# Optimization experiments

Hardware: AMD Instinct MI355X
Metric: run time of the kernel (lower is better)

Reference implementation:

```python
import jax, jax.numpy as jnp
import numpy as np

B, S = 1, 4096
H, KV, D, HID = 8, 4, 256, 2304   # heads, kv heads, head_dim, hidden_size
G = H // KV                        # GQA group size
WINDOW = 1024                      # sliding window
THETA = 10000.0                    # rope_local_base_freq (sliding attention)
EPS = 1e-6
SCALE = 256.0 ** -0.5              # query_pre_attn_scalar ** -0.5


def rms_norm(x, w, eps=EPS):
    # Gemma3RMSNorm: fp32 rms over last dim, scale by (1 + weight)
    v = jnp.mean(jnp.square(x), axis=-1, keepdims=True)
    return x * jax.lax.rsqrt(v + eps) * (1.0 + w)


def rope(x, position_ids):
    # x: [B, S, N, D]; split-half rotation as in Gemma3RotaryEmbedding
    d = x.shape[-1]
    inv_freq = 1.0 / (THETA ** (jnp.arange(0, d, 2, dtype=jnp.float32) / d))  # [D/2]
    freqs = position_ids.astype(jnp.float32)[:, :, None] * inv_freq  # [B, S, D/2]
    cos = jnp.cos(freqs)[:, :, None, :]  # [B, S, 1, D/2]
    sin = jnp.sin(freqs)[:, :, None, :]
    x1, x2 = jnp.split(x, 2, axis=-1)
    return jnp.concatenate([x1 * cos - x2 * sin, x1 * sin + x2 * cos], axis=-1)


def setup_inputs() -> dict:
    key = jax.random.key(0)
    ks = jax.random.split(key, 6)
    n = lambda k, shp, sc: jax.random.normal(k, shp, dtype=jnp.float32) * sc
    return {
        "x": n(ks[0], (B, S, HID), 1.0),
        "position_ids": jnp.broadcast_to(jnp.arange(S, dtype=jnp.int32)[None, :], (B, S)),
        "wq": n(ks[1], (HID, H * D), 0.02),
        "wk": n(ks[2], (HID, KV * D), 0.02),
        "wv": n(ks[3], (HID, KV * D), 0.02),
        "wo": n(ks[4], (H * D, HID), 0.02),
        "q_norm_w": jnp.zeros((D,), dtype=jnp.float32),
        "k_norm_w": jnp.zeros((D,), dtype=jnp.float32),
    }


def reference(x, position_ids, wq, wk, wv, wo, q_norm_w, k_norm_w):
    b, s, _ = x.shape
    q = (x @ wq).reshape(b, s, H, D)
    k = (x @ wk).reshape(b, s, KV, D)
    v = (x @ wv).reshape(b, s, KV, D)

    # QK-RMSNorm over head_dim, then RoPE, then query scaling
    q = rms_norm(q, q_norm_w)
    k = rms_norm(k, k_norm_w)
    q = rope(q, position_ids)
    k = rope(k, position_ids)
    q = q * SCALE

    # GQA: group queries over shared KV heads. qg: [B, S, KV, G, D]
    qg = q.reshape(b, s, KV, G, D)
    scores = jnp.einsum('bqcgd,btcd->bcgqt', qg, k)  # [B, KV, G, S, S]

    # causal + sliding-window mask: t <= q and q - t < WINDOW
    pi = position_ids[:, :, None]  # query positions [B, S, 1]
    pj = position_ids[:, None, :]  # key positions   [B, 1, S]
    mask = (pj <= pi) & (pi - pj < WINDOW)  # [B, S, S]
    neg = jnp.finfo(scores.dtype).min
    scores = jnp.where(mask[:, None, None, :, :], scores, neg)

    probs = jax.nn.softmax(scores, axis=-1)
    out = jnp.einsum('bcgqt,btcd->bqcgd', probs, v).reshape(b, s, H * D)
    return out @ wo
```

## Files before the change

### kernel.cpp

```cpp
#include <hip/hip_runtime.h>
#include <stdint.h>

typedef unsigned short u16;
typedef __attribute__((ext_vector_type(8))) short bf16x8;
typedef __attribute__((ext_vector_type(4))) float f32x4;

#define S_LEN 4096
#define HID_DIM 2304
#define QKV_N 4096
#define AO_N 2048
#define HD 256
#define WIN 1024
#define QSCALE 0.0625f

static __device__ __forceinline__ u16 f2bf(float f) {
  union { float f; uint32_t u; } v; v.f = f;
  return (u16)((v.u + 0x7FFFu + ((v.u >> 16) & 1u)) >> 16);
}
static __device__ __forceinline__ float bf2f(u16 h) {
  union { uint32_t u; float f; } v; v.u = ((uint32_t)h) << 16;
  return v.f;
}

static __device__ __forceinline__ void gld16(const void* src, void* dst) {
  __builtin_amdgcn_global_load_lds((const __attribute__((address_space(1))) void*)src,
                                   (__attribute__((address_space(3))) void*)dst, 16, 0, 0);
}

#define BAR() __builtin_amdgcn_s_barrier()
#define LG0() asm volatile("s_waitcnt lgkmcnt(0)" ::: "memory")
#define VM6() asm volatile("s_waitcnt vmcnt(6)" ::: "memory")
#define VM5() asm volatile("s_waitcnt vmcnt(5)" ::: "memory")
#define VM4() asm volatile("s_waitcnt vmcnt(4)" ::: "memory")
#define VM3() asm volatile("s_waitcnt vmcnt(3)" ::: "memory")
#define VM2() asm volatile("s_waitcnt vmcnt(2)" ::: "memory")
#define VM0() asm volatile("s_waitcnt vmcnt(0)" ::: "memory")
#define PRIO1() __builtin_amdgcn_s_setprio(1)
#define PRIO0() __builtin_amdgcn_s_setprio(0)

__global__ __launch_bounds__(256) void k_cvt_bf16(const float* __restrict__ in,
                                                  u16* __restrict__ out, int n) {
  int i = (blockIdx.x * 256 + threadIdx.x) * 4;
  if (i >= n) return;
  float4 v = *(const float4*)(in + i);
  uint64_t p = (uint64_t)f2bf(v.x) | ((uint64_t)f2bf(v.y) << 16)
             | ((uint64_t)f2bf(v.z) << 32) | ((uint64_t)f2bf(v.w) << 48);
  *(uint64_t*)(out + i) = p;
}

__global__ __launch_bounds__(256) void k_sincos(const int* __restrict__ pos_ids,
                                                float* __restrict__ ctab,
                                                float* __restrict__ stab) {
  int idx = blockIdx.x * 256 + threadIdx.x;
  int s = idx >> 7, j = idx & 127;
  float ang = (float)pos_ids[s] * exp2f((float)j * (-13.287712379549449f / 128.0f));
  float sn, c;
  sincosf(ang, &sn, &c);
  ctab[idx] = c;
  stab[idx] = sn;
}

__global__ __launch_bounds__(256) void k_transpose_cvt(const float* __restrict__ in, int C,
                                                       u16* __restrict__ out, int out_stride,
                                                       int row_off) {
  __shared__ float tile[32][33];
  int c0 = blockIdx.x * 32, r0 = blockIdx.y * 32;
  int tx = threadIdx.x & 31, ty = threadIdx.x >> 5;
#pragma unroll
  for (int i = 0; i < 4; i++)
    tile[ty + i * 8][tx] = in[(size_t)(r0 + ty + i * 8) * C + c0 + tx];
  __syncthreads();
#pragma unroll
  for (int i = 0; i < 4; i++)
    out[(size_t)(row_off + c0 + ty + i * 8) * out_stride + r0 + tx] = f2bf(tile[tx][ty + i * 8]);
}

__global__ __launch_bounds__(256) void k_transpose_w(const float* __restrict__ wq,
                                                     const float* __restrict__ wk,
                                                     const float* __restrict__ wv,
                                                     u16* __restrict__ out) {
  int ct = blockIdx.x;
  int r0 = blockIdx.y * 32;
  const float* src;
  int C, c0;
  if (ct < 64) {
    src = wq; C = 2048; c0 = ct * 32;
  } else if (ct < 96) {
    src = wk; C = 1024; c0 = (ct - 64) * 32;
  } else {
    src = wv; C = 1024; c0 = (ct - 96) * 32;
  }
  __shared__ float tile[32][33];
  int tx = threadIdx.x & 31, ty = threadIdx.x >> 5;
#pragma unroll
  for (int i = 0; i < 4; i++)
    tile[ty + i * 8][tx] = src[(size_t)(r0 + ty + i * 8) * C + c0 + tx];
  __syncthreads();
#pragma unroll
  for (int i = 0; i < 4; i++)
    out[(size_t)(ct * 32 + ty + i * 8) * HID_DIM + r0 + tx] = f2bf(tile[tx][ty + i * 8]);
}

template <int MODE>
__global__ __launch_bounds__(512, 2) void k_gemm8p(const u16* __restrict__ A,
                                                   const u16* __restrict__ Bt,
                                                   void* __restrict__ Cout,
                                                   int M, int N, int K,
                                                   const float* __restrict__ ctab,
                                                   const float* __restrict__ stab,
                                                   const float* __restrict__ qnw,
                                                   const float* __restrict__ knw,
                                                   u16* __restrict__ vtb) {
  __shared__ u16 sA[2][256 * 64];
  __shared__ u16 sB[2][256 * 64];
  const int t = threadIdx.x, lane = t & 63, wave = t >> 6;
  const int wr = wave >> 2, wc = wave & 3;
  const int l15 = lane & 15, l4 = lane >> 4;
  const int nbn = N >> 8;
  const int cpx = gridDim.x >> 3;
  const int wg = ((int)blockIdx.x & 7) * cpx + ((int)blockIdx.x >> 3);
  const int bm = wg / nbn, bn = wg % nbn;
  const int NT = K >> 6;
  const int srow = lane >> 3;
  const int sslot = ((lane & 7) ^ srow) * 8;
  const u16* Abase = A + (size_t)(bm * 256) * K;
  const u16* Bbase = Bt + (size_t)(bn * 256) * K;
  f32x4 acc[8][4] = {};
  bf16x8 aF[4][2], b01[2][2], b23[2][2];

#define STG_A(BUF, HALF, KT) do {                                                 \
    _Pragma("unroll")                                                             \
    for (int c_ = 0; c_ < 2; c_++) {                                              \
      int rb_ = (HALF) * 128 + (wave * 2 + c_) * 8;                               \
      gld16(Abase + (size_t)(rb_ + srow) * K + ((KT) << 6) + sslot,               \
            &sA[BUF][rb_ * 64]);                                                  \
    }                                                                             \
  } while (0)
#define STG_B(BUF, HALF, KT) do {                                                 \
    _Pragma("unroll")                                                             \
    for (int c_ = 0; c_ < 2; c_++) {                                              \
      int rb_ = (HALF) * 128 + (wave * 2 + c_) * 8;                               \
      gld16(Bbase + (size_t)(rb_ + srow) * K + ((KT) << 6) + sslot,               \
            &sB[BUF][rb_ * 64]);                                                  \
    }                                                                             \
  } while (0)
#define LDA(BUF, M_, KK)                                                          \
  (*(const bf16x8*)&sA[BUF][((M_) * 32 + wr * 16 + l15) * 64 +                    \
                            ((((KK) << 2) + l4) ^ (l15 & 7)) * 8])
#define LDB(BUF, N_, KK)                                                          \
  (*(const bf16x8*)&sB[BUF][((N_) * 64 + wc * 16 + l15) * 64 +                    \
                            ((((KK) << 2) + l4) ^ (l15 & 7)) * 8])

#define P1_LOADS(b_) do {                                                         \
    _Pragma("unroll") for (int m_ = 0; m_ < 4; m_++)                              \
      _Pragma("unroll") for (int k_ = 0; k_ < 2; k_++)                            \
        aF[m_][k_] = LDA(b_, m_, k_);                                             \
    _Pragma("unroll") for (int n_ = 0; n_ < 2; n_++)                              \
      _Pragma("unroll") for (int k_ = 0; k_ < 2; k_++)                            \
        b01[n_][k_] = LDB(b_, n_, k_);                                            \
  } while (0)
#define P2_LOADS(b_) do {                                                         \
    _Pragma("unroll") for (int n_ = 0; n_ < 2; n_++)                              \
      _Pragma("unroll") for (int k_ = 0; k_ < 2; k_++)                            \
        b23[n_][k_] = LDB(b_, n_ + 2, k_);                                        \
  } while (0)
#define P3_LOADS(b_) do {                                                         \
    _Pragma("unroll") for (int m_ = 0; m_ < 4; m_++)                              \
      _Pragma("unroll") for (int k_ = 0; k_ < 2; k_++)                            \
        aF[m_][k_] = LDA(b_, m_ + 4, k_);                                         \
  } while (0)
#define MFMA16(MOFF, NOFF, BREG) do {                                             \
    _Pragma("unroll") for (int m_ = 0; m_ < 4; m_++)                              \
      _Pragma("unroll") for (int n_ = 0; n_ < 2; n_++)                            \
        _Pragma("unroll") for (int k_ = 0; k_ < 2; k_++)                          \
          acc[m_ + MOFF][n_ + NOFF] = __builtin_amdgcn_mfma_f32_16x16x32_bf16(    \
              aF[m_][k_], BREG[n_][k_], acc[m_ + MOFF][n_ + NOFF], 0, 0, 0);      \
  } while (0)

  STG_A(0, 0, 0);
  STG_B(0, 0, 0);
  STG_B(0, 1, 0);
  STG_A(0, 1, 0);
  VM4();
  BAR();

  for (int tt = 0; tt < NT - 1; ++tt) {
    const int b = tt & 1, nb = b ^ 1;
    P1_LOADS(b);
    STG_A(nb, 0, tt + 1);
    STG_B(nb, 0, tt + 1);
    BAR(); LG0(); PRIO1(); MFMA16(0, 0, b01); PRIO0();
    VM6();
    BAR();
    P2_LOADS(b);
    STG_B(nb, 1, tt + 1);
    BAR(); LG0(); PRIO1(); MFMA16(0, 2, b23); PRIO0();
    VM6();
    BAR();
    P3_LOADS(b);
    STG_A(nb, 1, tt + 1);
    BAR(); LG0(); PRIO1(); MFMA16(4, 0, b01); PRIO0();
    BAR();
    PRIO1(); MFMA16(4, 2, b23); PRIO0();
    VM4();
    BAR();
  }
  {
    const int b = (NT - 1) & 1;
    P1_LOADS(b);
    BAR(); LG0(); PRIO1(); MFMA16(0, 0, b01); PRIO0();
    VM2();
    BAR();
    P2_LOADS(b);
    BAR(); LG0(); PRIO1(); MFMA16(0, 2, b23); PRIO0();
    VM0();
    BAR();
    P3_LOADS(b);
    BAR(); LG0(); PRIO1(); MFMA16(4, 0, b01); PRIO0();
    BAR();
    PRIO1(); MFMA16(4, 2, b23); PRIO0();
  }

  if (MODE == 1) {
    __syncthreads();
    float* slab = (float*)&sA[0][0];
    if (bn < 12) {
      const float* wvec = (bn < 8) ? qnw : knw;
      const float scl = (bn < 8) ? QSCALE : 1.0f;
      f32x4 wv4 = *(const f32x4*)&wvec[lane * 4];
#pragma unroll
      for (int m = 0; m < 8; m++) {
#pragma unroll
        for (int n = 0; n < 4; n++)
#pragma unroll
          for (int r = 0; r < 4; r++)
            slab[(wr * 16 + l4 * 4 + r) * 264 + n * 64 + wc * 16 + l15] = acc[m][n][r];
        __syncthreads();
#pragma unroll
        for (int rr = 0; rr < 4; rr++) {
          int lrow = wave * 4 + rr;
          int grow = bm * 256 + m * 32 + lrow;
          f32x4 v = *(const f32x4*)&slab[lrow * 264 + lane * 4];
          float ss = v[0] * v[0] + v[1] * v[1] + v[2] * v[2] + v[3] * v[3];
#pragma unroll
          for (int off = 1; off < 64; off <<= 1) ss += __shfl_xor(ss, off);
          float rms = rsqrtf(ss * (1.0f / 256.0f) + 1e-6f);
          float y[4], yo[4];
#pragma unroll
          for (int j = 0; j < 4; j++) y[j] = v[j] * rms * (1.0f + wv4[j]);
#pragma unroll
          for (int j = 0; j < 4; j++) yo[j] = __shfl_xor(y[j], 32);
          f32x4 cv = *(const f32x4*)&ctab[grow * 128 + (lane & 31) * 4];
          f32x4 sv = *(const f32x4*)&stab[grow * 128 + (lane & 31) * 4];
          uint64_t pk = 0;
#pragma unroll
          for (int j = 0; j < 4; j++) {
            float o = (lane < 32) ? (y[j] * cv[j] - yo[j] * sv[j])
                                  : (yo[j] * sv[j] + y[j] * cv[j]);
            pk |= (uint64_t)f2bf(o * scl) << (16 * j);
          }
          *(uint64_t*)&((u16*)Cout)[(size_t)grow * N + bn * 256 + lane * 4] = pk;
        }
        __syncthreads();
      }
    } else {
      const int kvh = bn - 12;
      const int d = t >> 1, sh = (t & 1) * 16;
#pragma unroll
      for (int m = 0; m < 8; m++) {
#pragma unroll
        for (int n = 0; n < 4; n++)
#pragma unroll
          for (int r = 0; r < 4; r++)
            slab[(wr * 16 + l4 * 4 + r) * 264 + n * 64 + wc * 16 + l15] = acc[m][n][r];
        __syncthreads();
        u16* dst = vtb + (size_t)(kvh * 256 + d) * S_LEN + bm * 256 + m * 32 + sh;
#pragma unroll
        for (int g = 0; g < 4; g++) {
          uint64_t pk = 0;
#pragma unroll
          for (int jj = 0; jj < 4; jj++)
            pk |= (uint64_t)f2bf(slab[(sh + g * 4 + jj) * 264 + d]) << (16 * jj);
          *(uint64_t*)(dst + g * 4) = pk;
        }
        __syncthreads();
      }
    }
  } else {
#pragma unroll
    for (int m = 0; m < 8; m++)
#pragma unroll
      for (int n = 0; n < 4; n++)
#pragma unroll
        for (int r = 0; r < 4; r++) {
          size_t row = bm * 256 + m * 32 + wr * 16 + l4 * 4 + r;
          size_t col = bn * 256 + n * 64 + wc * 16 + l15;
          ((float*)Cout)[row * N + col] = acc[m][n][r];
        }
  }
#undef STG_A
#undef STG_B
#undef LDA
#undef LDB
#undef P1_LOADS
#undef P2_LOADS
#undef P3_LOADS
#undef MFMA16
}

__global__ __launch_bounds__(512, 2) void k_gemm192(const u16* __restrict__ A,
                                                    const u16* __restrict__ Bt,
                                                    float* __restrict__ Cout,
                                                    int M, int N, int K) {
  __shared__ u16 sA[2][256 * 64];
  __shared__ u16 sB[2][192 * 64];
  const int t = threadIdx.x, lane = t & 63, wave = t >> 6;
  const int wr = wave >> 2, wc = wave & 3;
  const int l15 = lane & 15, l4 = lane >> 4;
  const int nbn = N / 192;
  const int cpx = gridDim.x >> 3;
  const int wg = ((int)blockIdx.x & 7) * cpx + ((int)blockIdx.x >> 3);
  const int bm = wg / nbn, bn = wg % nbn;
  const int NT = K >> 6;
  const int srow = lane >> 3;
  const int sslot = ((lane & 7) ^ srow) * 8;
  const u16* Abase = A + (size_t)(bm * 256) * K;
  const u16* Bbase = Bt + (size_t)(bn * 192) * K;
  f32x4 acc[8][3] = {};
  bf16x8 aF[4][2], b01[2][2], b2[2];

#define GA_STG_A(BUF, HALF, KT) do {                                              \
    _Pragma("unroll")                                                             \
    for (int c_ = 0; c_ < 2; c_++) {                                              \
      int rb_ = (HALF) * 128 + (wave * 2 + c_) * 8;                               \
      gld16(Abase + (size_t)(rb_ + srow) * K + ((KT) << 6) + sslot,               \
            &sA[BUF][rb_ * 64]);                                                  \
    }                                                                             \
  } while (0)
#define GA_STG_BC(BUF, CH, KT) do {                                               \
    int rb_ = (CH) * 64 + wave * 8;                                               \
    gld16(Bbase + (size_t)(rb_ + srow) * K + ((KT) << 6) + sslot,                 \
          &sB[BUF][rb_ * 64]);                                                    \
  } while (0)
#define GA_LDA(BUF, M_, KK)                                                       \
  (*(const bf16x8*)&sA[BUF][((M_) * 32 + wr * 16 + l15) * 64 +                    \
                            ((((KK) << 2) + l4) ^ (l15 & 7)) * 8])
#define GA_LDB(BUF, N_, KK)                                                       \
  (*(const bf16x8*)&sB[BUF][((N_) * 64 + wc * 16 + l15) * 64 +                    \
                            ((((KK) << 2) + l4) ^ (l15 & 7)) * 8])
#define GA_P1_LOADS(b_) do {                                                      \
    _Pragma("unroll") for (int m_ = 0; m_ < 4; m_++)                              \
      _Pragma("unroll") for (int k_ = 0; k_ < 2; k_++)                            \
        aF[m_][k_] = GA_LDA(b_, m_, k_);                                          \
    _Pragma("unroll") for (int n_ = 0; n_ < 2; n_++)                              \
      _Pragma("unroll") for (int k_ = 0; k_ < 2; k_++)                            \
        b01[n_][k_] = GA_LDB(b_, n_, k_);                                         \
  } while (0)
#define GA_P2_LOADS(b_) do {                                                      \
    _Pragma("unroll") for (int k_ = 0; k_ < 2; k_++)                              \
      b2[k_] = GA_LDB(b_, 2, k_);                                                 \
  } while (0)
#define GA_P3_LOADS(b_) do {                                                      \
    _Pragma("unroll") for (int m_ = 0; m_ < 4; m_++)                              \
      _Pragma("unroll") for (int k_ = 0; k_ < 2; k_++)                            \
        aF[m_][k_] = GA_LDA(b_, m_ + 4, k_);                                      \
  } while (0)
#define GA_MFMA_N01(MOFF) do {                                                    \
    _Pragma("unroll") for (int m_ = 0; m_ < 4; m_++)                              \
      _Pragma("unroll") for (int n_ = 0; n_ < 2; n_++)                            \
        _Pragma("unroll") for (int k_ = 0; k_ < 2; k_++)                          \
          acc[m_ + MOFF][n_] = __builtin_amdgcn_mfma_f32_16x16x32_bf16(           \
              aF[m_][k_], b01[n_][k_], acc[m_ + MOFF][n_], 0, 0, 0);              \
  } while (0)
#define GA_MFMA_N2(MOFF) do {                                                     \
    _Pragma("unroll") for (int m_ = 0; m_ < 4; m_++)                              \
      _Pragma("unroll") for (int k_ = 0; k_ < 2; k_++)                            \
        acc[m_ + MOFF][2] = __builtin_amdgcn_mfma_f32_16x16x32_bf16(              \
            aF[m_][k_], b2[k_], acc[m_ + MOFF][2], 0, 0, 0);                      \
  } while (0)

  GA_STG_A(0, 0, 0);
  GA_STG_BC(0, 0, 0);
  GA_STG_BC(0, 1, 0);
  GA_STG_BC(0, 2, 0);
  GA_STG_A(0, 1, 0);
  VM3();
  BAR();

  for (int tt = 0; tt < NT - 1; ++tt) {
    const int b = tt & 1, nb = b ^ 1;
    GA_P1_LOADS(b);
    GA_STG_A(nb, 0, tt + 1);
    GA_STG_BC(nb, 0, tt + 1);
    GA_STG_BC(nb, 1, tt + 1);
    BAR(); LG0(); PRIO1(); GA_MFMA_N01(0); PRIO0();
    VM6();
    BAR();
    GA_P2_LOADS(b);
    GA_STG_BC(nb, 2, tt + 1);
    BAR(); LG0(); PRIO1(); GA_MFMA_N2(0); PRIO0();
    VM5();
    BAR();
    GA_P3_LOADS(b);
    GA_STG_A(nb, 1, tt + 1);
    BAR(); LG0(); PRIO1(); GA_MFMA_N01(4); PRIO0();
    BAR();
    PRIO1(); GA_MFMA_N2(4); PRIO0();
    VM3();
    BAR();
  }
  {
    const int b = (NT - 1) & 1;
    GA_P1_LOADS(b);
    BAR(); LG0(); PRIO1(); GA_MFMA_N01(0); PRIO0();
    VM2();
    BAR();
    GA_P2_LOADS(b);
    BAR(); LG0(); PRIO1(); GA_MFMA_N2(0); PRIO0();
    VM0();
    BAR();
    GA_P3_LOADS(b);
    BAR(); LG0(); PRIO1(); GA_MFMA_N01(4); PRIO0();
    BAR();
    PRIO1(); GA_MFMA_N2(4); PRIO0();
  }

#pragma unroll
  for (int m = 0; m < 8; m++)
#pragma unroll
    for (int n = 0; n < 3; n++)
#pragma unroll
      for (int r = 0; r < 4; r++) {
        size_t row = bm * 256 + m * 32 + wr * 16 + l4 * 4 + r;
        size_t col = bn * 192 + n * 64 + wc * 16 + l15;
        Cout[row * N + col] = acc[m][n][r];
      }
#undef GA_STG_A
#undef GA_STG_BC
#undef GA_LDA
#undef GA_LDB
#undef GA_P1_LOADS
#undef GA_P2_LOADS
#undef GA_P3_LOADS
#undef GA_MFMA_N01
#undef GA_MFMA_N2
}

__global__ __launch_bounds__(512, 2) void k_attn(const u16* __restrict__ qkv,
                                                 const u16* __restrict__ vt,
                                                 const int* __restrict__ pos_ids,
                                                 u16* __restrict__ aout) {
  __shared__ u16 lK[2][64 * 256];
  __shared__ u16 lV[2][256 * 64];
  __shared__ u16 lP[8][16 * 64];
  const int bid = blockIdx.x;
  const int wg = (bid & 7) * 32 + (bid >> 3);
  const int kvh = wg >> 6;
  const int q0 = (wg & 63) * 64;
  const int t = threadIdx.x, lane = t & 63, wave = t >> 6;
  const int l15 = lane & 15, l4 = lane >> 4;
  const int head = kvh * 2 + (wave >> 2);
  const int qw = q0 + (wave & 3) * 16;

  bf16x8 qfr[8];
  {
    const u16* qptr = qkv + (size_t)(qw + l15) * QKV_N + head * HD + l4 * 8;
#pragma unroll
    for (int kc = 0; kc < 8; kc++) qfr[kc] = *(const bf16x8*)(qptr + kc * 32);
  }
  f32x4 acc[16] = {};
  float mrow[4], lrow[4];
#pragma unroll
  for (int r = 0; r < 4; r++) { mrow[r] = -1e30f; lrow[r] = 0.0f; }
  int qi[4];
#pragma unroll
  for (int r = 0; r < 4; r++) qi[r] = pos_ids[qw + l4 * 4 + r];

  const int krw = lane >> 5, kcl = lane & 31;
  const int vrw = lane >> 3, vcl = lane & 7;
  const u16* kgb = qkv + 2048 + kvh * HD;
  const u16* vgb = vt + (size_t)kvh * HD * S_LEN;

  int start = q0 - (WIN - 1);
  if (start < 0) start = 0;
  start &= ~63;

#define STAGE_KV(B, T0) do {                                                          \
    _Pragma("unroll")                                                                 \
    for (int i_ = 0; i_ < 4; i_++) {                                                  \
      int ch_ = wave * 4 + i_;                                                        \
      int kr_ = ch_ * 2 + krw;                                                        \
      gld16(kgb + (size_t)((T0) + kr_) * QKV_N + ((kcl ^ (kr_ & 7)) * 8),             \
            &lK[B][ch_ * 512]);                                                       \
      int vr_ = ch_ * 8 + vrw;                                                        \
      gld16(vgb + (size_t)vr_ * S_LEN + (T0) + ((vcl ^ (vr_ & 7)) * 8),               \
            &lV[B][ch_ * 512]);                                                       \
    }                                                                                 \
  } while (0)

  STAGE_KV(0, start);
  __syncthreads();
  int buf = 0;
  for (int t0 = start; t0 <= q0 + 63; t0 += 64) {
    if (t0 + 64 <= q0 + 63) STAGE_KV(buf ^ 1, t0 + 64);
    int kp[4];
#pragma unroll
    for (int kb = 0; kb < 4; kb++) kp[kb] = pos_ids[t0 + kb * 16 + l15];
    f32x4 sv[4] = {};
    PRIO1();
#pragma unroll
    for (int kb = 0; kb < 4; kb++) {
      const char* krow = (const char*)&lK[buf][(kb * 16 + l15) * 256];
      const int sw = ((kb * 16 + l15) & 7) << 4;
#pragma unroll
      for (int kc = 0; kc < 8; kc++) {
        bf16x8 kf = *(const bf16x8*)(krow + ((kc * 64 + l4 * 16) ^ sw));
        sv[kb] = __builtin_amdgcn_mfma_f32_16x16x32_bf16(qfr[kc], kf, sv[kb], 0, 0, 0);
      }
    }
    PRIO0();
    float sloc[4][4], mx[4];
    float need = 0.0f;
#pragma unroll
    for (int r = 0; r < 4; r++) {
      int pi = qi[r];
#pragma unroll
      for (int kb = 0; kb < 4; kb++)
        sloc[r][kb] = ((kp[kb] <= pi) && (pi - kp[kb] < WIN)) ? sv[kb][r] : -__builtin_inff();
      float m_ = fmaxf(fmaxf(sloc[r][0], sloc[r][1]), fmaxf(sloc[r][2], sloc[r][3]));
#pragma unroll
      for (int off = 1; off < 16; off <<= 1) m_ = fmaxf(m_, __shfl_xor(m_, off));
      mx[r] = m_;
      need = fmaxf(need, m_ - mrow[r]);
    }
    bool resc = __any(need > 8.0f);
    if (resc) {
#pragma unroll
      for (int r = 0; r < 4; r++) {
        float nm = fmaxf(mrow[r], mx[r]);
        float al = __expf(mrow[r] - nm);
        mrow[r] = nm;
        lrow[r] *= al;
#pragma unroll
        for (int nd = 0; nd < 16; nd++) acc[nd][r] *= al;
      }
    }
#pragma unroll
    for (int r = 0; r < 4; r++) {
      float nm = mrow[r];
      float e0 = __expf(sloc[r][0] - nm), e1 = __expf(sloc[r][1] - nm);
      float e2 = __expf(sloc[r][2] - nm), e3 = __expf(sloc[r][3] - nm);
      float sum = (e0 + e1) + (e2 + e3);
#pragma unroll
      for (int off = 1; off < 16; off <<= 1) sum += __shfl_xor(sum, off);
      lrow[r] += sum;
      int q = l4 * 4 + r;
      char* lpw = (char*)&lP[wave][0] + q * 128;
      int swp = (q & 7) << 4;
      *(u16*)(lpw + ((l15 * 2) ^ swp)) = f2bf(e0);
      *(u16*)(lpw + ((32 + l15 * 2) ^ swp)) = f2bf(e1);
      *(u16*)(lpw + ((64 + l15 * 2) ^ swp)) = f2bf(e2);
      *(u16*)(lpw + ((96 + l15 * 2) ^ swp)) = f2bf(e3);
    }
#pragma unroll
    for (int kc2 = 0; kc2 < 2; kc2++) {
      int q = l15;
      bf16x8 pa = *(const bf16x8*)((const char*)&lP[wave][0] + q * 128 +
                                   ((kc2 * 64 + l4 * 16) ^ ((q & 7) << 4)));
      PRIO1();
#pragma unroll
      for (int nd = 0; nd < 16; nd++) {
        int d = nd * 16 + l15;
        bf16x8 vf = *(const bf16x8*)((const char*)&lV[buf][d * 64] +
                                     ((kc2 * 64 + l4 * 16) ^ ((d & 7) << 4)));
        acc[nd] = __builtin_amdgcn_mfma_f32_16x16x32_bf16(pa, vf, acc[nd], 0, 0, 0);
      }
      PRIO0();
    }
    __syncthreads();
    buf ^= 1;
  }
  float rinv[4];
#pragma unroll
  for (int r = 0; r < 4; r++) rinv[r] = 1.0f / lrow[r];
#pragma unroll
  for (int nd = 0; nd < 16; nd++)
#pragma unroll
    for (int r = 0; r < 4; r++) {
      size_t row = qw + l4 * 4 + r;
      aout[row * AO_N + head * HD + nd * 16 + l15] = f2bf(acc[nd][r] * rinv[r]);
    }
#undef STAGE_KV
}

extern "C" void kernel_launch(void* const* d_in, const int* in_sizes, int n_in,
                              void* d_out, int out_size, void* d_ws, size_t ws_size,
                              hipStream_t stream) {
  const float* x = (const float*)d_in[0];
  const int* pos = (const int*)d_in[1];
  const float* wq = (const float*)d_in[2];
  const float* wk = (const float*)d_in[3];
  const float* wv = (const float*)d_in[4];
  const float* wo = (const float*)d_in[5];
  const float* qnw = (const float*)d_in[6];
  const float* knw = (const float*)d_in[7];

  u16* qkv = (u16*)d_out;
  float* ctab = (float*)((char*)d_out + 33554432);
  float* stab = (float*)((char*)d_out + 35651584);
  u16* xbf = (u16*)d_ws;
  u16* wT = (u16*)((char*)d_ws + 18874368);
  u16* vtb = (u16*)((char*)d_ws + 28311552);
  u16* aout = xbf;

  k_cvt_bf16<<<9216, 256, 0, stream>>>(x, xbf, S_LEN * HID_DIM);
  k_sincos<<<2048, 256, 0, stream>>>(pos, ctab, stab);
  k_transpose_w<<<dim3(128, 72), 256, 0, stream>>>(wq, wk, wv, wT);
  k_gemm8p<1><<<dim3(256), 512, 0, stream>>>(xbf, wT, qkv, S_LEN, QKV_N, HID_DIM,
                                             ctab, stab, qnw, knw, vtb);
  k_transpose_cvt<<<dim3(72, 64), 256, 0, stream>>>(wo, HID_DIM, wT, 2048, 0);
  k_attn<<<dim3(256), 512, 0, stream>>>(qkv, vtb, pos, aout);
  k_gemm192<<<dim3(192), 512, 0, stream>>>(aout, wT, (float*)d_out, S_LEN, HID_DIM, 2048);
}
```

Measured before the change: 229.9 us.

## Remap GEMM tiles to XCDs as 2D blocks and widen epilogue slabs

Measured after the change: 226.7 us (median of 3 runs). No clear change (-1.4%).

```diff
diff --git a/kernel.cpp b/kernel.cpp
--- a/kernel.cpp
+++ b/kernel.cpp
@@ -111,15 +111,24 @@
                                                    const float* __restrict__ qnw,
                                                    const float* __restrict__ knw,
                                                    u16* __restrict__ vtb) {
-  __shared__ u16 sA[2][256 * 64];
-  __shared__ u16 sB[2][256 * 64];
+  __shared__ u16 sAB[4 * 256 * 64];
   const int t = threadIdx.x, lane = t & 63, wave = t >> 6;
   const int wr = wave >> 2, wc = wave & 3;
   const int l15 = lane & 15, l4 = lane >> 4;
   const int nbn = N >> 8;
-  const int cpx = gridDim.x >> 3;
-  const int wg = ((int)blockIdx.x & 7) * cpx + ((int)blockIdx.x >> 3);
-  const int bm = wg / nbn, bn = wg % nbn;
+  int bm, bn;
+  {
+    const int xcd = (int)blockIdx.x & 7, loc = (int)blockIdx.x >> 3;
+    if (nbn == 16) {
+      bm = (xcd >> 1) * 4 + (loc >> 3);
+      bn = (xcd & 1) * 8 + (loc & 7);
+    } else {
+      const int cpx = gridDim.x >> 3;
+      const int wg = xcd * cpx + loc;
+      bm = wg / nbn;
+      bn = wg % nbn;
+    }
+  }
   const int NT = K >> 6;
   const int srow = lane >> 3;
   const int sslot = ((lane & 7) ^ srow) * 8;
@@ -128,12 +137,14 @@
   f32x4 acc[8][4] = {};
   bf16x8 aF[4][2], b01[2][2], b23[2][2];
 
+#define SA_(b) (&sAB[(b) * 16384])
+#define SB_(b) (&sAB[32768 + (b) * 16384])
 #define STG_A(BUF, HALF, KT) do {                                                 \
     _Pragma("unroll")                                                             \
     for (int c_ = 0; c_ < 2; c_++) {                                              \
       int rb_ = (HALF) * 128 + (wave * 2 + c_) * 8;                               \
       gld16(Abase + (size_t)(rb_ + srow) * K + ((KT) << 6) + sslot,               \
-            &sA[BUF][rb_ * 64]);                                                  \
+            SA_(BUF) + rb_ * 64);                                                 \
     }                                                                             \
   } while (0)
 #define STG_B(BUF, HALF, KT) do {                                                 \
@@ -141,15 +152,15 @@
     for (int c_ = 0; c_ < 2; c_++) {                                              \
       int rb_ = (HALF) * 128 + (wave * 2 + c_) * 8;                               \
       gld16(Bbase + (size_t)(rb_ + srow) * K + ((KT) << 6) + sslot,               \
-            &sB[BUF][rb_ * 64]);                                                  \
+            SB_(BUF) + rb_ * 64);                                                 \
     }                                                                             \
   } while (0)
 #define LDA(BUF, M_, KK)                                                          \
-  (*(const bf16x8*)&sA[BUF][((M_) * 32 + wr * 16 + l15) * 64 +                    \
-                            ((((KK) << 2) + l4) ^ (l15 & 7)) * 8])
+  (*(const bf16x8*)&SA_(BUF)[((M_) * 32 + wr * 16 + l15) * 64 +                   \
+                             ((((KK) << 2) + l4) ^ (l15 & 7)) * 8])
 #define LDB(BUF, N_, KK)                                                          \
-  (*(const bf16x8*)&sB[BUF][((N_) * 64 + wc * 16 + l15) * 64 +                    \
-                            ((((KK) << 2) + l4) ^ (l15 & 7)) * 8])
+  (*(const bf16x8*)&SB_(BUF)[((N_) * 64 + wc * 16 + l15) * 64 +                   \
+                             ((((KK) << 2) + l4) ^ (l15 & 7)) * 8])
 
 #define P1_LOADS(b_) do {                                                         \
     _Pragma("unroll") for (int m_ = 0; m_ < 4; m_++)                              \
@@ -223,23 +234,28 @@
 
   if (MODE == 1) {
     __syncthreads();
-    float* slab = (float*)&sA[0][0];
+    float* slab = (float*)sAB;
     if (bn < 12) {
       const float* wvec = (bn < 8) ? qnw : knw;
       const float scl = (bn < 8) ? QSCALE : 1.0f;
       f32x4 wv4 = *(const f32x4*)&wvec[lane * 4];
 #pragma unroll
-      for (int m = 0; m < 8; m++) {
-#pragma unroll
-        for (int n = 0; n < 4; n++)
-#pragma unroll
-          for (int r = 0; r < 4; r++)
-            slab[(wr * 16 + l4 * 4 + r) * 264 + n * 64 + wc * 16 + l15] = acc[m][n][r];
+      for (int mp = 0; mp < 4; mp++) {
+#pragma unroll
+        for (int mh = 0; mh < 2; mh++) {
+          int m = mp * 2 + mh;
+#pragma unroll
+          for (int n = 0; n < 4; n++)
+#pragma unroll
+            for (int r = 0; r < 4; r++)
+              slab[(mh * 32 + wr * 16 + l4 * 4 + r) * 264 + n * 64 + wc * 16 + l15] =
+                  acc[m][n][r];
+        }
         __syncthreads();
 #pragma unroll
-        for (int rr = 0; rr < 4; rr++) {
-          int lrow = wave * 4 + rr;
-          int grow = bm * 256 + m * 32 + lrow;
+        for (int rr = 0; rr < 8; rr++) {
+          int lrow = wave * 8 + rr;
+          int grow = bm * 256 + mp * 64 + lrow;
           f32x4 v = *(const f32x4*)&slab[lrow * 264 + lane * 4];
           float ss = v[0] * v[0] + v[1] * v[1] + v[2] * v[2] + v[3] * v[3];
 #pragma unroll
@@ -265,23 +281,29 @@
       }
     } else {
       const int kvh = bn - 12;
-      const int d = t >> 1, sh = (t & 1) * 16;
-#pragma unroll
-      for (int m = 0; m < 8; m++) {
-#pragma unroll
-        for (int n = 0; n < 4; n++)
-#pragma unroll
-          for (int r = 0; r < 4; r++)
-            slab[(wr * 16 + l4 * 4 + r) * 264 + n * 64 + wc * 16 + l15] = acc[m][n][r];
+      const int dcol = wave * 32 + (lane >> 1);
+      const int shalf = (lane & 1) * 32;
+#pragma unroll
+      for (int mp = 0; mp < 4; mp++) {
+#pragma unroll
+        for (int mh = 0; mh < 2; mh++) {
+          int m = mp * 2 + mh;
+#pragma unroll
+          for (int n = 0; n < 4; n++)
+#pragma unroll
+            for (int r = 0; r < 4; r++)
+              slab[(mh * 32 + wr * 16 + l4 * 4 + r) * 264 + n * 64 + wc * 16 + l15] =
+                  acc[m][n][r];
+        }
         __syncthreads();
-        u16* dst = vtb + (size_t)(kvh * 256 + d) * S_LEN + bm * 256 + m * 32 + sh;
+        u16* dst = vtb + (size_t)(kvh * 256 + dcol) * S_LEN + bm * 256 + mp * 64 + shalf;
 #pragma unroll
         for (int g = 0; g < 4; g++) {
-          uint64_t pk = 0;
-#pragma unroll
-          for (int jj = 0; jj < 4; jj++)
-            pk |= (uint64_t)f2bf(slab[(sh + g * 4 + jj) * 264 + d]) << (16 * jj);
-          *(uint64_t*)(dst + g * 4) = pk;
+          u16 tmp[8];
+#pragma unroll
+          for (int jj = 0; jj < 8; jj++)
+            tmp[jj] = f2bf(slab[(shalf + g * 8 + jj) * 264 + dcol]);
+          *(bf16x8*)(dst + g * 8) = *(const bf16x8*)tmp;
         }
         __syncthreads();
       }
@@ -298,6 +320,8 @@
           ((float*)Cout)[row * N + col] = acc[m][n][r];
         }
   }
+#undef SA_
+#undef SB_
 #undef STG_A
 #undef STG_B
 #undef LDA
@@ -317,10 +341,9 @@
   const int t = threadIdx.x, lane = t & 63, wave = t >> 6;
   const int wr = wave >> 2, wc = wave & 3;
   const int l15 = lane & 15, l4 = lane >> 4;
-  const int nbn = N / 192;
-  const int cpx = gridDim.x >> 3;
-  const int wg = ((int)blockIdx.x & 7) * cpx + ((int)blockIdx.x >> 3);
-  const int bm = wg / nbn, bn = wg % nbn;
+  const int xcd = (int)blockIdx.x & 7, loc = (int)blockIdx.x >> 3;
+  const int bm = (xcd >> 1) * 4 + loc / 6;
+  const int bn = (xcd & 1) * 6 + loc % 6;
   const int NT = K >> 6;
   const int srow = lane >> 3;
   const int sslot = ((lane & 7) ^ srow) * 8;
```
